# Performance work log

Measured on AMD Instinct MI355X. Metric: run time of the kernel, lower is better.

Reference implementation:

```python
import jax, jax.numpy as jnp
import numpy as np
import math

B, S, D, H, M, R = 4, 1024, 1024, 16, 4, 64
DH = D // H
EPS = 1e-8

def setup_inputs() -> dict:
    key = jax.random.key(0)
    ks = jax.random.split(key, 8)
    sc = 0.02
    return {
        'x': jax.random.normal(ks[0], (B, S, D), jnp.float32),
        'Wk': jax.random.normal(ks[1], (D, D), jnp.float32) * sc,
        'bk': jnp.zeros((D,), jnp.float32),
        'Wq': jax.random.normal(ks[2], (D, D), jnp.float32) * sc,
        'bq': jnp.zeros((D,), jnp.float32),
        'Wv': jax.random.normal(ks[3], (D, D), jnp.float32) * sc,
        'bv': jnp.zeros((D,), jnp.float32),
        'mask1': jax.random.normal(ks[4], (M, R, S), jnp.float32) * sc,
        'mask2': jax.random.normal(ks[5], (M, R, S), jnp.float32) * sc,
        'roll_back': jax.random.randint(ks[6], (M, S, S), 0, S, jnp.int64),
    }

def reference(x, Wk, bk, Wq, bq, Wv, bv, mask1, mask2, roll_back):
    def proj(W, b):
        # torch Linear: x @ W^T + b ; reshape to [B, H, S, DH]
        y = jnp.dot(x, W.T) + b
        return y.reshape(B, S, H, DH).transpose(0, 2, 1, 3)
    k = proj(Wk, bk)
    q = proj(Wq, bq)
    v = proj(Wv, bv)
    # learnable low-rank mask: [M, S, S]
    learnable_mask = jnp.einsum('mrs,mrt->mst', mask1, mask2)
    # gather along last dim with roll_back indices
    gathered = jnp.take_along_axis(learnable_mask, roll_back, axis=-1)  # [M, S, S]
    att = jnp.einsum('bhsd,bhtd->bhst', q, k) / math.sqrt(DH)  # [B, H, S, S]
    att = att.reshape(B, H // M, M, S, S) * gathered[None, None]
    att = att.reshape(B, H, S, S)
    # Frobenius norm over last two dims per (B, H)
    fro = jnp.sqrt(jnp.sum(att * att, axis=(-2, -1), keepdims=True))
    att = att / (fro + EPS)
    out = jnp.einsum('bhst,bhtd->bhsd', att, v)
    return out.transpose(0, 2, 1, 3).reshape(B, S, D)
```

## Files before the change

### kernel.cpp

```cpp
#include <hip/hip_runtime.h>
#include <hip/hip_bf16.h>
#include <stdint.h>

typedef __attribute__((ext_vector_type(8))) __bf16 bf16x8;
typedef __attribute__((ext_vector_type(4))) float  f32x4;
typedef __attribute__((ext_vector_type(16))) float f32x16;

__device__ __forceinline__ ushort f2bf(float f) {
    union { float f; uint32_t u; } v; v.f = f;
    uint32_t u = v.u;
    uint32_t r = 0x7FFFu + ((u >> 16) & 1u);
    return (ushort)((u + r) >> 16);
}
__device__ __forceinline__ float bf2f(ushort u) {
    union { uint32_t u; float f; } v; v.u = ((uint32_t)u) << 16;
    return v.f;
}

typedef __attribute__((address_space(3))) uint32_t lds_u32_t;
typedef const __attribute__((address_space(1))) uint32_t glb_u32_t;
__device__ __forceinline__ void async_copy16(const void* g, void* l) {
    __builtin_amdgcn_global_load_lds((glb_u32_t*)g, (lds_u32_t*)l, 16, 0, 0);
}

__global__ __launch_bounds__(256) void convert_all(
    const float* __restrict__ x, const float* __restrict__ wk,
    const float* __restrict__ wq, const float* __restrict__ wv,
    ushort* __restrict__ xb, ushort* __restrict__ wball)
{
    int i = blockIdx.x * 256 + threadIdx.x;
    const float* src; ushort* dst; int j;
    if (i < 1048576) { src = x; dst = xb; j = i; }
    else {
        int t = i - 1048576;
        int z = t >> 18;
        j = t & 262143;
        src = (z == 0) ? wk : (z == 1) ? wq : wv;
        dst = wball + z * 1048576;
    }
    float4 f = ((const float4*)src)[j];
    ushort4 o;
    o.x = f2bf(f.x); o.y = f2bf(f.y); o.z = f2bf(f.z); o.w = f2bf(f.w);
    ((ushort4*)dst)[j] = o;
}

__global__ __launch_bounds__(256) void proj_gemm(
    const ushort* __restrict__ xb, const ushort* __restrict__ wball,
    const float* __restrict__ bk, const float* __restrict__ bq, const float* __restrict__ bv,
    ushort* __restrict__ kd, ushort* __restrict__ qd, ushort* __restrict__ vd)
{
    __shared__ ushort As[128 * 32];
    __shared__ ushort Bs[128 * 32];
    const int z = blockIdx.z;
    const int row0 = blockIdx.x * 128;
    const int col0 = blockIdx.y * 128;
    const ushort* wb = wball + z * 1048576;
    const int tid = threadIdx.x;
    const int lane = tid & 63, wave = tid >> 6;
    const int quad = lane >> 4, m15 = lane & 15;
    const int wr = wave >> 1, wc = wave & 1;

    f32x4 acc[4][4];
    for (int i = 0; i < 4; i++)
        for (int j = 0; j < 4; j++) acc[i][j] = (f32x4){0.f, 0.f, 0.f, 0.f};

    for (int kk = 0; kk < 1024; kk += 32) {
        __syncthreads();
        #pragma unroll
        for (int i = 0; i < 2; i++) {
            int c = tid + i * 256;
            int r = c >> 2, off = (c & 3) * 8;
            async_copy16(&xb[(row0 + r) * 1024 + kk + off], &As[c * 8]);
            async_copy16(&wb[(col0 + r) * 1024 + kk + off], &Bs[c * 8]);
        }
        __syncthreads();
        bf16x8 af[4], bfv[4];
        #pragma unroll
        for (int fr = 0; fr < 4; fr++)
            af[fr] = *(const bf16x8*)&As[(wr * 64 + fr * 16 + m15) * 32 + quad * 8];
        #pragma unroll
        for (int fc = 0; fc < 4; fc++)
            bfv[fc] = *(const bf16x8*)&Bs[(wc * 64 + fc * 16 + m15) * 32 + quad * 8];
        #pragma unroll
        for (int fr = 0; fr < 4; fr++)
            #pragma unroll
            for (int fc = 0; fc < 4; fc++)
                acc[fr][fc] = __builtin_amdgcn_mfma_f32_16x16x32_bf16(af[fr], bfv[fc], acc[fr][fc], 0, 0, 0);
    }

    const float* bias = (z == 0) ? bk : (z == 1) ? bq : bv;
    ushort* dstA = (z == 0) ? kd : qd;
    for (int fr = 0; fr < 4; fr++) {
        int ibase = row0 + wr * 64 + fr * 16 + quad * 4;
        int b_ = ibase >> 10, s = ibase & 1023;
        for (int fc = 0; fc < 4; fc++) {
            int j = col0 + wc * 64 + fc * 16 + m15;
            int h = j >> 6, dh = j & 63;
            float bb = bias[j];
            if (z < 2) {
                for (int r = 0; r < 4; r++)
                    dstA[((b_ * 16 + h) * 1024 + (s + r)) * 64 + dh] = f2bf(acc[fr][fc][r] + bb);
            } else {
                ushort4 o;
                o.x = f2bf(acc[fr][fc][0] + bb);
                o.y = f2bf(acc[fr][fc][1] + bb);
                o.z = f2bf(acc[fr][fc][2] + bb);
                o.w = f2bf(acc[fr][fc][3] + bb);
                *(ushort4*)&vd[((b_ * 16 + h) * 64 + dh) * 1024 + s] = o;
            }
        }
    }
}

__global__ __launch_bounds__(256) void mask_lr(const float* __restrict__ m1,
                                               const float* __restrict__ m2,
                                               float* __restrict__ lm)
{
    __shared__ float As[64 * 64];
    __shared__ float Bs2[64 * 64];
    const int m = blockIdx.z;
    const int s0 = blockIdx.x * 64, u0 = blockIdx.y * 64;
    const int tid = threadIdx.x;
    for (int i = 0; i < 4; i++) {
        int c = tid + i * 256;
        int r = c >> 4, off = (c & 15) * 4;
        *(float4*)&As[r * 64 + off]  = *(const float4*)&m1[(m * 64 + r) * 1024 + s0 + off];
        *(float4*)&Bs2[r * 64 + off] = *(const float4*)&m2[(m * 64 + r) * 1024 + u0 + off];
    }
    __syncthreads();
    const int tx = tid & 15, ty = tid >> 4;
    float acc[4][4] = {};
    for (int r = 0; r < 64; r++) {
        float4 a = *(const float4*)&As[r * 64 + ty * 4];
        float4 b = *(const float4*)&Bs2[r * 64 + tx * 4];
        float aa[4] = {a.x, a.y, a.z, a.w}, bb[4] = {b.x, b.y, b.z, b.w};
        for (int i = 0; i < 4; i++)
            for (int j = 0; j < 4; j++) acc[i][j] += aa[i] * bb[j];
    }
    for (int i = 0; i < 4; i++) {
        float4 o = {acc[i][0], acc[i][1], acc[i][2], acc[i][3]};
        *(float4*)&lm[(m * 1024 + s0 + ty * 4 + i) * 1024 + u0 + tx * 4] = o;
    }
}

__global__ __launch_bounds__(256) void mask_gather(const float* __restrict__ lm,
                                                   const int* __restrict__ rb,
                                                   ushort* __restrict__ gth)
{
    __shared__ float row[1024];
    const int s = blockIdx.x, m = blockIdx.y;
    const int tid = threadIdx.x;
    const int base = (m * 1024 + s) * 1024;
    *(float4*)&row[tid * 4] = *(const float4*)&lm[base + tid * 4];
    __syncthreads();
    int4 idx = ((const int4*)(rb + base))[tid];
    ushort4 o;
    o.x = f2bf(row[idx.x & 1023] * 0.125f);
    o.y = f2bf(row[idx.y & 1023] * 0.125f);
    o.z = f2bf(row[idx.z & 1023] * 0.125f);
    o.w = f2bf(row[idx.w & 1023] * 0.125f);
    ((ushort4*)(gth + base))[tid] = o;
}

__global__ __launch_bounds__(256, 2) void attention(
    const ushort* __restrict__ qd, const ushort* __restrict__ kd, const ushort* __restrict__ vd,
    const ushort* __restrict__ gth, float* __restrict__ O, float* __restrict__ ss)
{
    __shared__ ushort Ks[64 * 72];
    __shared__ ushort Vs[64 * 72];
    __shared__ ushort Ps[64 * 72];
    __shared__ ushort Ms[64 * 72];
    __shared__ float red[4];
    const int s0 = blockIdx.x * 64;
    const int bh = blockIdx.y;
    const int mm = bh & 3;
    const int tid = threadIdx.x, lane = tid & 63, wave = tid >> 6;
    const int l31 = lane & 31, hl = lane >> 5;
    const int wr2 = wave >> 1, wc2 = wave & 1;

    #pragma unroll
    for (int i = 0; i < 2; i++) {
        int c = tid + i * 256;
        int r = c >> 3, off = (c & 7) * 8;
        *(uint4*)&Ms[r * 72 + off] = *(const uint4*)&qd[(bh * 1024 + s0 + r) * 64 + off];
    }
    __syncthreads();
    bf16x8 qf[4];
    #pragma unroll
    for (int kk = 0; kk < 4; kk++)
        qf[kk] = *(const bf16x8*)&Ms[(wr2 * 32 + l31) * 72 + kk * 16 + hl * 8];

    f32x16 oacc;
    #pragma unroll
    for (int i = 0; i < 16; i++) oacc[i] = 0.f;
    float ssacc = 0.f;
    const ushort* gbase = gth + mm * 1048576 + s0 * 1024;

    for (int t0 = 0; t0 < 1024; t0 += 64) {
        __syncthreads();
        #pragma unroll
        for (int i = 0; i < 2; i++) {
            int c = tid + i * 256;
            int r = c >> 3, off = (c & 7) * 8;
            *(uint4*)&Ks[r * 72 + off] = *(const uint4*)&kd[(bh * 1024 + t0 + r) * 64 + off];
            *(uint4*)&Vs[r * 72 + off] = *(const uint4*)&vd[(bh * 64 + r) * 1024 + t0 + off];
            *(uint4*)&Ms[r * 72 + off] = *(const uint4*)&gbase[r * 1024 + t0 + off];
        }
        __syncthreads();

        f32x16 p;
        #pragma unroll
        for (int i = 0; i < 16; i++) p[i] = 0.f;
        #pragma unroll
        for (int kk = 0; kk < 4; kk++) {
            bf16x8 b = *(const bf16x8*)&Ks[(wc2 * 32 + l31) * 72 + kk * 16 + hl * 8];
            p = __builtin_amdgcn_mfma_f32_32x32x16_bf16(qf[kk], b, p, 0, 0, 0);
        }
        {
            const int col = wc2 * 32 + l31;
            #pragma unroll
            for (int reg = 0; reg < 16; reg++) {
                int row = wr2 * 32 + (reg & 3) + 8 * (reg >> 2) + 4 * hl;
                float pv = p[reg] * bf2f(Ms[row * 72 + col]);
                ssacc += pv * pv;
                Ps[row * 72 + col] = f2bf(pv);
            }
        }
        __syncthreads();
        #pragma unroll
        for (int kk = 0; kk < 4; kk++) {
            bf16x8 a = *(const bf16x8*)&Ps[(wr2 * 32 + l31) * 72 + kk * 16 + hl * 8];
            bf16x8 b = *(const bf16x8*)&Vs[(wc2 * 32 + l31) * 72 + kk * 16 + hl * 8];
            oacc = __builtin_amdgcn_mfma_f32_32x32x16_bf16(a, b, oacc, 0, 0, 0);
        }
    }
    #pragma unroll
    for (int reg = 0; reg < 16; reg++) {
        int s = s0 + wr2 * 32 + (reg & 3) + 8 * (reg >> 2) + 4 * hl;
        int dh = wc2 * 32 + l31;
        O[(bh * 1024 + s) * 64 + dh] = oacc[reg];
    }
    for (int off = 32; off; off >>= 1) ssacc += __shfl_down(ssacc, off, 64);
    if (lane == 0) red[wave] = ssacc;
    __syncthreads();
    if (tid == 0) atomicAdd(&ss[bh], red[0] + red[1] + red[2] + red[3]);
}

__global__ __launch_bounds__(256) void normalize_out(const float* __restrict__ O,
                                                     const float* __restrict__ ss,
                                                     float* __restrict__ out)
{
    int gid = blockIdx.x * 256 + threadIdx.x;
    int e = gid * 4;
    int bh = e >> 16;
    float inv = 1.f / (sqrtf(ss[bh]) + 1e-8f);
    float4 v4 = *(const float4*)&O[e];
    int b_ = bh >> 4, h = bh & 15;
    int s = (e >> 6) & 1023, dh = e & 63;
    float4 o4 = {v4.x * inv, v4.y * inv, v4.z * inv, v4.w * inv};
    *(float4*)&out[((b_ * 1024 + s) * 16 + h) * 64 + dh] = o4;
}

extern "C" void kernel_launch(void* const* d_in, const int* in_sizes, int n_in,
                              void* d_out, int out_size, void* d_ws, size_t ws_size,
                              hipStream_t stream) {
    const float* x  = (const float*)d_in[0];
    const float* Wk = (const float*)d_in[1];
    const float* bk = (const float*)d_in[2];
    const float* Wq = (const float*)d_in[3];
    const float* bq = (const float*)d_in[4];
    const float* Wv = (const float*)d_in[5];
    const float* bv = (const float*)d_in[6];
    const float* m1 = (const float*)d_in[7];
    const float* m2 = (const float*)d_in[8];
    const int*   rb = (const int*)d_in[9];
    float* out = (float*)d_out;

    char* ws = (char*)d_ws;
    ushort* xb    = (ushort*)(ws);
    ushort* wball = (ushort*)(ws + 8388608);
    ushort* kd    = (ushort*)(ws + 14680064);
    ushort* qd    = (ushort*)(ws + 23068672);
    ushort* vd    = (ushort*)(ws + 31457280);
    float*  lm    = (float*)(ws + 39845888);
    ushort* gth   = (ushort*)(ws + 56623104);
    float*  ssb   = (float*)(ws + 65011712);

    convert_all<<<7168, 256, 0, stream>>>(x, Wk, Wq, Wv, xb, wball);
    proj_gemm<<<dim3(32, 8, 3), 256, 0, stream>>>(xb, wball, bk, bq, bv, kd, qd, vd);
    mask_lr<<<dim3(16, 16, 4), 256, 0, stream>>>(m1, m2, lm);
    mask_gather<<<dim3(1024, 4), 256, 0, stream>>>(lm, rb, gth);
    hipMemsetAsync(ssb, 0, 64 * sizeof(float), stream);
    float* O = lm;
    attention<<<dim3(16, 64), 256, 0, stream>>>(qd, kd, vd, gth, O, ssb);
    normalize_out<<<4096, 256, 0, stream>>>(O, ssb, out);
}
```

Before: 214.6 us.

## Fuse low-rank mask build with gather; widen and swizzle proj GEMM K-tile

Merges the low-rank mask product and the roll-back gather into one kernel. Each block computes 8 rows of the learnable mask into shared memory and gathers from it directly, so the 16 MB fp32 mask is never written to or read back from global memory. The projection GEMM now loads 64-wide K tiles with an XOR swizzle on the LDS layout. This halves the K-loop iterations and barriers and aims to avoid LDS bank conflicts. Each mask block re-reads all of m2 from global memory (likely cache-resident), and the larger LDS tiles may reduce occupancy.

After: 204.4 us. 1.05x faster.

```diff
diff --git a/kernel.cpp b/kernel.cpp
--- a/kernel.cpp
+++ b/kernel.cpp
@@ -49,8 +49,8 @@
     const float* __restrict__ bk, const float* __restrict__ bq, const float* __restrict__ bv,
     ushort* __restrict__ kd, ushort* __restrict__ qd, ushort* __restrict__ vd)
 {
-    __shared__ ushort As[128 * 32];
-    __shared__ ushort Bs[128 * 32];
+    __shared__ ushort As[128 * 64];
+    __shared__ ushort Bs[128 * 64];
     const int z = blockIdx.z;
     const int row0 = blockIdx.x * 128;
     const int col0 = blockIdx.y * 128;
@@ -64,28 +64,38 @@
     for (int i = 0; i < 4; i++)
         for (int j = 0; j < 4; j++) acc[i][j] = (f32x4){0.f, 0.f, 0.f, 0.f};
 
-    for (int kk = 0; kk < 1024; kk += 32) {
-        __syncthreads();
-        #pragma unroll
-        for (int i = 0; i < 2; i++) {
+    for (int kk = 0; kk < 1024; kk += 64) {
+        __syncthreads();
+        #pragma unroll
+        for (int i = 0; i < 4; i++) {
             int c = tid + i * 256;
-            int r = c >> 2, off = (c & 3) * 8;
-            async_copy16(&xb[(row0 + r) * 1024 + kk + off], &As[c * 8]);
-            async_copy16(&wb[(col0 + r) * 1024 + kk + off], &Bs[c * 8]);
-        }
-        __syncthreads();
-        bf16x8 af[4], bfv[4];
-        #pragma unroll
-        for (int fr = 0; fr < 4; fr++)
-            af[fr] = *(const bf16x8*)&As[(wr * 64 + fr * 16 + m15) * 32 + quad * 8];
-        #pragma unroll
-        for (int fc = 0; fc < 4; fc++)
-            bfv[fc] = *(const bf16x8*)&Bs[(wc * 64 + fc * 16 + m15) * 32 + quad * 8];
-        #pragma unroll
-        for (int fr = 0; fr < 4; fr++)
+            int r = c >> 3, cjp = c & 7;
+            int cj = cjp ^ (r & 7);
+            async_copy16(&xb[(row0 + r) * 1024 + kk + cj * 8], &As[c * 8]);
+            async_copy16(&wb[(col0 + r) * 1024 + kk + cj * 8], &Bs[c * 8]);
+        }
+        __syncthreads();
+        #pragma unroll
+        for (int kh = 0; kh < 2; kh++) {
+            bf16x8 af[4], bfv[4];
             #pragma unroll
-            for (int fc = 0; fc < 4; fc++)
-                acc[fr][fc] = __builtin_amdgcn_mfma_f32_16x16x32_bf16(af[fr], bfv[fc], acc[fr][fc], 0, 0, 0);
+            for (int fr = 0; fr < 4; fr++) {
+                int row = wr * 64 + fr * 16 + m15;
+                int q4 = kh * 4 + quad;
+                af[fr] = *(const bf16x8*)&As[row * 64 + ((q4 ^ (row & 7)) * 8)];
+            }
+            #pragma unroll
+            for (int fc = 0; fc < 4; fc++) {
+                int row = wc * 64 + fc * 16 + m15;
+                int q4 = kh * 4 + quad;
+                bfv[fc] = *(const bf16x8*)&Bs[row * 64 + ((q4 ^ (row & 7)) * 8)];
+            }
+            #pragma unroll
+            for (int fr = 0; fr < 4; fr++)
+                #pragma unroll
+                for (int fc = 0; fc < 4; fc++)
+                    acc[fr][fc] = __builtin_amdgcn_mfma_f32_16x16x32_bf16(af[fr], bfv[fc], acc[fr][fc], 0, 0, 0);
+        }
     }
 
     const float* bias = (z == 0) ? bk : (z == 1) ? bq : bv;
@@ -112,54 +122,55 @@
     }
 }
 
-__global__ __launch_bounds__(256) void mask_lr(const float* __restrict__ m1,
-                                               const float* __restrict__ m2,
-                                               float* __restrict__ lm)
-{
-    __shared__ float As[64 * 64];
-    __shared__ float Bs2[64 * 64];
-    const int m = blockIdx.z;
-    const int s0 = blockIdx.x * 64, u0 = blockIdx.y * 64;
+__global__ __launch_bounds__(256) void mask_fused(
+    const float* __restrict__ m1, const float* __restrict__ m2,
+    const int* __restrict__ rb, ushort* __restrict__ gth)
+{
+    __shared__ float As8[64 * 8];
+    __shared__ float lmS[8 * 1024];
+    const int s0 = blockIdx.x * 8;
+    const int m = blockIdx.y;
     const int tid = threadIdx.x;
-    for (int i = 0; i < 4; i++) {
+
+    if (tid < 128) {
+        int r = tid >> 1, half = tid & 1;
+        *(float4*)&As8[r * 8 + half * 4] =
+            *(const float4*)&m1[(m * 64 + r) * 1024 + s0 + half * 4];
+    }
+    __syncthreads();
+
+    f32x4 acc8[8];
+    #pragma unroll
+    for (int s = 0; s < 8; s++) acc8[s] = (f32x4){0.f, 0.f, 0.f, 0.f};
+    const float* m2b = m2 + m * 65536 + tid * 4;
+    #pragma unroll 4
+    for (int r = 0; r < 64; r++) {
+        float4 b4 = *(const float4*)&m2b[r * 1024];
+        f32x4 b = (f32x4){b4.x, b4.y, b4.z, b4.w};
+        #pragma unroll
+        for (int s = 0; s < 8; s++) {
+            float a = As8[r * 8 + s];
+            acc8[s] += a * b;
+        }
+    }
+    #pragma unroll
+    for (int s = 0; s < 8; s++)
+        *(f32x4*)&lmS[s * 1024 + tid * 4] = acc8[s];
+    __syncthreads();
+
+    const int base = (m * 1024 + s0) * 1024;
+    #pragma unroll
+    for (int i = 0; i < 8; i++) {
         int c = tid + i * 256;
-        int r = c >> 4, off = (c & 15) * 4;
-        *(float4*)&As[r * 64 + off]  = *(const float4*)&m1[(m * 64 + r) * 1024 + s0 + off];
-        *(float4*)&Bs2[r * 64 + off] = *(const float4*)&m2[(m * 64 + r) * 1024 + u0 + off];
-    }
-    __syncthreads();
-    const int tx = tid & 15, ty = tid >> 4;
-    float acc[4][4] = {};
-    for (int r = 0; r < 64; r++) {
-        float4 a = *(const float4*)&As[r * 64 + ty * 4];
-        float4 b = *(const float4*)&Bs2[r * 64 + tx * 4];
-        float aa[4] = {a.x, a.y, a.z, a.w}, bb[4] = {b.x, b.y, b.z, b.w};
-        for (int i = 0; i < 4; i++)
-            for (int j = 0; j < 4; j++) acc[i][j] += aa[i] * bb[j];
-    }
-    for (int i = 0; i < 4; i++) {
-        float4 o = {acc[i][0], acc[i][1], acc[i][2], acc[i][3]};
-        *(float4*)&lm[(m * 1024 + s0 + ty * 4 + i) * 1024 + u0 + tx * 4] = o;
-    }
-}
-
-__global__ __launch_bounds__(256) void mask_gather(const float* __restrict__ lm,
-                                                   const int* __restrict__ rb,
-                                                   ushort* __restrict__ gth)
-{
-    __shared__ float row[1024];
-    const int s = blockIdx.x, m = blockIdx.y;
-    const int tid = threadIdx.x;
-    const int base = (m * 1024 + s) * 1024;
-    *(float4*)&row[tid * 4] = *(const float4*)&lm[base + tid * 4];
-    __syncthreads();
-    int4 idx = ((const int4*)(rb + base))[tid];
-    ushort4 o;
-    o.x = f2bf(row[idx.x & 1023] * 0.125f);
-    o.y = f2bf(row[idx.y & 1023] * 0.125f);
-    o.z = f2bf(row[idx.z & 1023] * 0.125f);
-    o.w = f2bf(row[idx.w & 1023] * 0.125f);
-    ((ushort4*)(gth + base))[tid] = o;
+        int row = c >> 8, j = (c & 255) * 4;
+        int4 idx = *(const int4*)&rb[base + row * 1024 + j];
+        ushort4 o;
+        o.x = f2bf(lmS[row * 1024 + (idx.x & 1023)] * 0.125f);
+        o.y = f2bf(lmS[row * 1024 + (idx.y & 1023)] * 0.125f);
+        o.z = f2bf(lmS[row * 1024 + (idx.z & 1023)] * 0.125f);
+        o.w = f2bf(lmS[row * 1024 + (idx.w & 1023)] * 0.125f);
+        *(ushort4*)&gth[base + row * 1024 + j] = o;
+    }
 }
 
 __global__ __launch_bounds__(256, 2) void attention(
@@ -282,16 +293,14 @@
     ushort* kd    = (ushort*)(ws + 14680064);
     ushort* qd    = (ushort*)(ws + 23068672);
     ushort* vd    = (ushort*)(ws + 31457280);
-    float*  lm    = (float*)(ws + 39845888);
+    float*  O     = (float*)(ws + 39845888);
     ushort* gth   = (ushort*)(ws + 56623104);
     float*  ssb   = (float*)(ws + 65011712);
 
     convert_all<<<7168, 256, 0, stream>>>(x, Wk, Wq, Wv, xb, wball);
     proj_gemm<<<dim3(32, 8, 3), 256, 0, stream>>>(xb, wball, bk, bq, bv, kd, qd, vd);
-    mask_lr<<<dim3(16, 16, 4), 256, 0, stream>>>(m1, m2, lm);
-    mask_gather<<<dim3(1024, 4), 256, 0, stream>>>(lm, rb, gth);
+    mask_fused<<<dim3(128, 4), 256, 0, stream>>>(m1, m2, rb, gth);
     hipMemsetAsync(ssb, 0, 64 * sizeof(float), stream);
-    float* O = lm;
     attention<<<dim3(16, 64), 256, 0, stream>>>(qd, kd, vd, gth, O, ssb);
     normalize_out<<<4096, 256, 0, stream>>>(O, ssb, out);
 }
```
